# Optimization experiments

Hardware: AMD Instinct MI355X
Metric: run time of the kernel (lower is better)

Reference implementation:

```python
import jax, jax.numpy as jnp
import numpy as np

B, S, D = 1, 2048, 4096
HQ, HK, HD = 32, 8, 128


def setup_inputs() -> dict:
    key = jax.random.key(0)
    ks = jax.random.split(key, 6)
    x = jax.random.normal(ks[0], (B, S, D), jnp.float32) * 0.02
    wq = jax.random.normal(ks[1], (D, HQ * HD), jnp.float32) * 0.02
    wk = jax.random.normal(ks[2], (D, HK * HD), jnp.float32) * 0.02
    wv = jax.random.normal(ks[3], (D, HK * HD), jnp.float32) * 0.02
    wo = jax.random.normal(ks[4], (HQ * HD, D), jnp.float32) * 0.02
    # canonical RoPE frequencies: theta = 10000
    inv_freq = 1.0 / (10000.0 ** (jnp.arange(0, HD, 2, dtype=jnp.float32) / HD))  # [HD/2]
    t = jnp.arange(S, dtype=jnp.float32)
    ang = jnp.outer(t, inv_freq)  # [S, HD/2]
    return {
        "x": x,
        "freqs_cos": jnp.cos(ang),
        "freqs_sin": jnp.sin(ang),
        "wq": wq, "wk": wk, "wv": wv, "wo": wo,
    }


def _rope(t, cos, sin):
    # t: [B, S, H, HD]; pairs are consecutive elements (view_as_complex semantics)
    tr = t.reshape(*t.shape[:-1], HD // 2, 2)
    t0, t1 = tr[..., 0], tr[..., 1]
    c = cos[None, :, None, :]
    s = sin[None, :, None, :]
    o0 = t0 * c - t1 * s
    o1 = t0 * s + t1 * c
    return jnp.stack([o0, o1], axis=-1).reshape(t.shape)


def reference(x, freqs_cos, freqs_sin, wq, wk, wv, wo):
    b, s, _ = x.shape
    g = HQ // HK  # GQA group size
    xq = (x @ wq).reshape(b, s, HQ, HD)
    xk = (x @ wk).reshape(b, s, HK, HD)
    xv = (x @ wv).reshape(b, s, HK, HD)
    xq = _rope(xq, freqs_cos, freqs_sin)
    xk = _rope(xk, freqs_cos, freqs_sin)
    scale = 1.0 / jnp.sqrt(jnp.float32(HD))
    xqg = xq.reshape(b, s, HK, g, HD)
    # scores: [b, HK, g, s_q, s_k]
    scores = jnp.einsum("bqkgd,bnkd->bkgqn", xqg, xk) * scale
    causal = jnp.tril(jnp.ones((s, s), dtype=bool))
    scores = jnp.where(causal[None, None, None, :, :], scores, -jnp.inf)
    p = jax.nn.softmax(scores, axis=-1)
    out = jnp.einsum("bkgqn,bnkd->bqkgd", p, xv).reshape(b, s, HQ * HD)
    return out @ wo
```

## Files before the change

kernel.cpp:

```cpp
#include <hip/hip_runtime.h>
#include <stdint.h>

typedef __bf16 bf16_t;
typedef bf16_t bf16x8 __attribute__((ext_vector_type(8)));
typedef float f32x4 __attribute__((ext_vector_type(4)));
typedef unsigned int u32;
typedef unsigned short u16;

#define DEV_INLINE __device__ __forceinline__

#define S_LEN 2048
#define D_MODEL 4096
#define HQ 32
#define HK 8
#define HD 128
#define NQKV 6144

DEV_INLINE u16 f2bf(float x) {
  union { float f; uint32_t u; } v; v.f = x;
  uint32_t r = v.u + 0x7FFFu + ((v.u >> 16) & 1u);
  return (u16)(r >> 16);
}
DEV_INLINE float bf2f(u16 x) {
  union { uint32_t u; float f; } v; v.u = ((uint32_t)x) << 16;
  return v.f;
}
DEV_INLINE u32 pack2bf(float a, float b) {
  return (u32)f2bf(a) | ((u32)f2bf(b) << 16);
}

DEV_INLINE void async_load16(const void* g, void* l) {
  __builtin_amdgcn_global_load_lds(
      (const __attribute__((address_space(1))) u32*)g,
      (__attribute__((address_space(3))) u32*)l, 16, 0, 0);
}

DEV_INLINE f32x4 mfma16(bf16x8 a, bf16x8 b, f32x4 c) {
  return __builtin_amdgcn_mfma_f32_16x16x32_bf16(a, b, c, 0, 0, 0);
}

__global__ void cvt_f32_bf16(const float* __restrict__ in, u16* __restrict__ out, int n) {
  int i = (blockIdx.x * blockDim.x + threadIdx.x) * 4;
  if (i >= n) return;
  float4 v = *(const float4*)(in + i);
  union { u16 s[4]; uint2 u; } o;
  o.s[0] = f2bf(v.x); o.s[1] = f2bf(v.y); o.s[2] = f2bf(v.z); o.s[3] = f2bf(v.w);
  *(uint2*)(out + i) = o.u;
}

__global__ void transpose_f32_bf16(const float* __restrict__ in, u16* __restrict__ out,
                                   int R, int C) {
  __shared__ float tile[32][33];
  int tx = threadIdx.x, ty = threadIdx.y;
  int c0 = blockIdx.x * 32, r0 = blockIdx.y * 32;
#pragma unroll
  for (int i = 0; i < 4; ++i)
    tile[ty + i * 8][tx] = in[(long)(r0 + ty + i * 8) * C + c0 + tx];
  __syncthreads();
#pragma unroll
  for (int i = 0; i < 4; ++i)
    out[(long)(c0 + ty + i * 8) * R + r0 + tx] = f2bf(tile[tx][ty + i * 8]);
}

__global__ void transpose_bf16(const u16* __restrict__ in, u16* __restrict__ out,
                               int R, int C, int ld_in, int col_off) {
  __shared__ u16 tile[32][33];
  int tx = threadIdx.x, ty = threadIdx.y;
  int c0 = blockIdx.x * 32, r0 = blockIdx.y * 32;
#pragma unroll
  for (int i = 0; i < 4; ++i)
    tile[ty + i * 8][tx] = in[(long)(r0 + ty + i * 8) * ld_in + col_off + c0 + tx];
  __syncthreads();
#pragma unroll
  for (int i = 0; i < 4; ++i)
    out[(long)(c0 + ty + i * 8) * R + r0 + tx] = tile[tx][ty + i * 8];
}

__global__ void rope_bf16(const u16* __restrict__ in, const float* __restrict__ cosb,
                          const float* __restrict__ sinb, u16* __restrict__ out,
                          int H, int ld_in, int col_off, float scale) {
  int idx = blockIdx.x * blockDim.x + threadIdx.x;
  int j = idx & 63;
  int sh = idx >> 6;
  int s = sh / H, h = sh - s * H;
  const u16* ip = in + (long)s * ld_in + col_off + h * HD;
  union { u32 u; u16 s2[2]; } v; v.u = *(const u32*)(ip + 2 * j);
  float q0 = bf2f(v.s2[0]), q1 = bf2f(v.s2[1]);
  float c = cosb[s * 64 + j], sn = sinb[s * 64 + j];
  union { u16 s2[2]; u32 u; } o;
  o.s2[0] = f2bf((q0 * c - q1 * sn) * scale);
  o.s2[1] = f2bf((q0 * sn + q1 * c) * scale);
  *(u32*)(out + (long)sh * HD + 2 * j) = o.u;
}

#define BARRIER() asm volatile("s_barrier" ::: "memory")
#define WAIT_LGKM0()                                            \
  do {                                                          \
    asm volatile("s_waitcnt lgkmcnt(0)" ::: "memory");          \
    __builtin_amdgcn_sched_barrier(0);                          \
  } while (0)
#define WAIT_VM(N) asm volatile("s_waitcnt vmcnt(" #N ")" ::: "memory")

#define PHASE_A(T, DO_STAGE)                                                      \
  {                                                                               \
    const u16* Ab_ = &lds[(T) & 3][0];                                            \
    const u16* Bb_ = &lds[(T) & 3][8192];                                         \
    bf16x8 af_[MFH];                                                              \
    _Pragma("unroll")                                                             \
    for (int i = 0; i < MFH; ++i) af_[i] = rdfrag(Ab_, wr * MROWS + i * 16 + l15);\
    _Pragma("unroll")                                                             \
    for (int j = 0; j < 4; ++j) bfr[j] = rdfrag(Bb_, wc * 64 + j * 16 + l15);     \
    if (DO_STAGE) stageA((T) + 3);                                                \
    BARRIER();                                                                    \
    WAIT_LGKM0();                                                                 \
    __builtin_amdgcn_s_setprio(1);                                                \
    _Pragma("unroll")                                                             \
    for (int i = 0; i < MFH; ++i)                                                 \
      _Pragma("unroll")                                                           \
      for (int j = 0; j < 4; ++j) acc[i][j] = mfma16(af_[i], bfr[j], acc[i][j]);  \
    __builtin_amdgcn_s_setprio(0);                                                \
    BARRIER();                                                                    \
  }

#define PHASE_B(T, DO_STAGE, VMWAIT)                                              \
  {                                                                               \
    const u16* Ab_ = &lds[(T) & 3][0];                                            \
    bf16x8 af_[MFH];                                                              \
    _Pragma("unroll")                                                             \
    for (int i = 0; i < MFH; ++i)                                                 \
      af_[i] = rdfrag(Ab_, wr * MROWS + (MFH + i) * 16 + l15);                    \
    if (DO_STAGE) stageB((T) + 3);                                                \
    BARRIER();                                                                    \
    WAIT_LGKM0();                                                                 \
    __builtin_amdgcn_s_setprio(1);                                                \
    _Pragma("unroll")                                                             \
    for (int i = 0; i < MFH; ++i)                                                 \
      _Pragma("unroll")                                                           \
      for (int j = 0; j < 4; ++j)                                                 \
        acc[MFH + i][j] = mfma16(af_[i], bfr[j], acc[MFH + i][j]);                \
    __builtin_amdgcn_s_setprio(0);                                                \
    VMWAIT;                                                                       \
    BARRIER();                                                                    \
  }

template <int BN, int WM, bool BF16OUT>
__global__ __launch_bounds__(512, 2) void gemm_pipe(
    const u16* __restrict__ A, const u16* __restrict__ Bt, void* __restrict__ Cv,
    int N, int K) {
  constexpr int WN = 8 / WM;
  constexpr int MROWS = 256 / WM;
  constexpr int MF = MROWS / 16;
  constexpr int MFH = MF / 2;
  constexpr int BPT = (BN * 4) / 512;
  constexpr int LDSU = (256 + BN) * 32;

  __shared__ __attribute__((aligned(16))) u16 lds[4][LDSU];

  const int tid = threadIdx.x;
  const int lane = tid & 63;
  const int wave = tid >> 6;
  const int quad = lane >> 4, l15 = lane & 15;
  const int wr = wave / WN, wc = wave % WN;

  const int gx = gridDim.x;
  const int bid = blockIdx.y * gx + blockIdx.x;
  const int cpx = (gx * gridDim.y) >> 3;
  const int sw = (bid & 7) * cpx + (bid >> 3);
  const int bn = sw % gx, bm = sw / gx;

  const long arow = (long)bm * 256, brow = (long)bn * BN;
  const int NT = K >> 5;

  auto stageA = [&](int ts) {
    const int bs = ts & 3;
    const int k0 = ts * 32;
#pragma unroll
    for (int j = 0; j < 2; ++j) {
      int c = tid + j * 512;
      int row = c >> 2, cc = c & 3, cs = cc ^ ((row >> 1) & 3);
      async_load16(A + (arow + row) * (long)K + k0 + cs * 8,
                   (u16*)&lds[bs][0] + c * 8);
    }
  };
  auto stageB = [&](int ts) {
    const int bs = ts & 3;
    const int k0 = ts * 32;
#pragma unroll
    for (int j = 0; j < BPT; ++j) {
      int c = tid + j * 512;
      int row = c >> 2, cc = c & 3, cs = cc ^ ((row >> 1) & 3);
      async_load16(Bt + (brow + row) * (long)K + k0 + cs * 8,
                   (u16*)&lds[bs][8192] + c * 8);
    }
  };
  auto rdfrag = [&](const u16* base, int row) -> bf16x8 {
    return *(const bf16x8*)(base + row * 32 + ((quad ^ ((row >> 1) & 3)) * 8));
  };

  f32x4 acc[MF][4] = {};
  bf16x8 bfr[4];

  stageA(0); stageB(0); stageA(1); stageB(1); stageA(2); stageB(2);
  if constexpr (BN == 256) { WAIT_VM(8); } else { WAIT_VM(6); }
  BARRIER();

  int t = 0;
  for (; t < NT - 3; ++t) {
    PHASE_A(t, true);
    if constexpr (BN == 256) { PHASE_B(t, true, WAIT_VM(8)); }
    else                     { PHASE_B(t, true, WAIT_VM(6)); }
  }
  PHASE_A(t, false);
  if constexpr (BN == 256) { PHASE_B(t, false, WAIT_VM(4)); }
  else                     { PHASE_B(t, false, WAIT_VM(3)); }
  ++t;
  PHASE_A(t, false);
  PHASE_B(t, false, WAIT_VM(0));
  ++t;
  PHASE_A(t, false);
  PHASE_B(t, false, ((void)0));

#pragma unroll
  for (int i = 0; i < MF; ++i) {
    const long row = (long)bm * 256 + wr * MROWS + i * 16 + quad * 4;
#pragma unroll
    for (int j = 0; j < 4; ++j) {
      const int col = bn * BN + wc * 64 + j * 16 + l15;
      if constexpr (BF16OUT) {
        u16* C = (u16*)Cv;
#pragma unroll
        for (int r = 0; r < 4; ++r) C[(row + r) * N + col] = f2bf(acc[i][j][r]);
      } else {
        float* C = (float*)Cv;
#pragma unroll
        for (int r = 0; r < 4; ++r) C[(row + r) * N + col] = acc[i][j][r];
      }
    }
  }
}

#define NEG_INF -1e30f
__global__ __launch_bounds__(256, 2) void attn_fwd(
    const u16* __restrict__ Qb, const u16* __restrict__ Kb,
    const u16* __restrict__ Vt, u16* __restrict__ Ob) {
  __shared__ __attribute__((aligned(16))) u16 Ks[128 * 128];
  __shared__ __attribute__((aligned(16))) u16 Vs[128 * 128];
  __shared__ __attribute__((aligned(16))) u16 Pts[4][16 * 128];
  const int tid = threadIdx.x;
  const int lane = tid & 63, wave = tid >> 6;
  const int quad = lane >> 4, l15 = lane & 15;
  const int u = 15 - blockIdx.x;
  const int h = blockIdx.y, hk = h >> 2;
  const int swz = 2 * (l15 & 7);

  bf16x8 qf[2][4];
#pragma unroll
  for (int n = 0; n < 2; ++n) {
    const u16* qrow = Qb + (long)(u * 128 + wave * 32 + n * 16 + l15) * (HQ * HD)
                      + h * HD + quad * 8;
#pragma unroll
    for (int ks = 0; ks < 4; ++ks) qf[n][ks] = *(const bf16x8*)(qrow + ks * 32);
  }

  float m_run[2] = {NEG_INF, NEG_INF}, l_run[2] = {0.f, 0.f};
  f32x4 oacc[8][2] = {};

  for (int j = 0; j <= u; ++j) {
#pragma unroll
    for (int it = 0; it < 8; ++it) {
      int c = tid + it * 256;
      int row = c >> 4, cc = c & 15, csrc = cc ^ (row & 15);
      async_load16(Kb + (long)(j * 128 + row) * (HK * HD) + hk * HD + csrc * 8,
                   (u16*)Ks + c * 8);
      async_load16(Vt + (long)(hk * HD + row) * S_LEN + j * 128 + csrc * 8,
                   (u16*)Vs + c * 8);
    }
    __syncthreads();

    f32x4 sc[8][2] = {};
#pragma unroll
    for (int ks = 0; ks < 4; ++ks)
#pragma unroll
      for (int tj = 0; tj < 8; ++tj) {
        int row = tj * 16 + l15;
        bf16x8 kf = *(const bf16x8*)(Ks + row * 128 + (((ks * 4 + quad) ^ (row & 15)) * 8));
        sc[tj][0] = mfma16(kf, qf[0][ks], sc[tj][0]);
        sc[tj][1] = mfma16(kf, qf[1][ks], sc[tj][1]);
      }

    const bool diag = (j == u);
#pragma unroll
    for (int n = 0; n < 2; ++n) {
      int qloc = wave * 32 + n * 16 + l15;
      if (diag) {
#pragma unroll
        for (int tj = 0; tj < 8; ++tj)
#pragma unroll
          for (int r = 0; r < 4; ++r)
            if (tj * 16 + quad * 4 + r > qloc) sc[tj][n][r] = NEG_INF;
      }
      float m = NEG_INF;
#pragma unroll
      for (int tj = 0; tj < 8; ++tj)
#pragma unroll
        for (int r = 0; r < 4; ++r) m = fmaxf(m, sc[tj][n][r]);
      m = fmaxf(m, __shfl_xor(m, 16));
      m = fmaxf(m, __shfl_xor(m, 32));
      float mnew = fmaxf(m_run[n], m);
      float alpha = __expf(m_run[n] - mnew);
      m_run[n] = mnew;
      float rs = 0.f;
#pragma unroll
      for (int tj = 0; tj < 8; ++tj)
#pragma unroll
        for (int r = 0; r < 4; ++r) {
          float p = __expf(sc[tj][n][r] - mnew);
          sc[tj][n][r] = p;
          rs += p;
        }
      rs += __shfl_xor(rs, 16);
      rs += __shfl_xor(rs, 32);
      l_run[n] = l_run[n] * alpha + rs;
#pragma unroll
      for (int tj = 0; tj < 8; ++tj) oacc[tj][n] *= alpha;
    }

    u16* pw = &Pts[wave][0];
    bf16x8 pf0[4], pf1[4];
#pragma unroll
    for (int tj = 0; tj < 8; ++tj) {
      union { u32 w[2]; uint2 u2; } pk;
      pk.w[0] = pack2bf(sc[tj][0][0], sc[tj][0][1]);
      pk.w[1] = pack2bf(sc[tj][0][2], sc[tj][0][3]);
      *(uint2*)(pw + l15 * 128 + (((tj * 4 + quad) ^ swz) * 4)) = pk.u2;
    }
    __asm__ volatile("s_waitcnt lgkmcnt(0)" ::: "memory");
#pragma unroll
    for (int ks = 0; ks < 4; ++ks)
      pf0[ks] = *(const bf16x8*)(pw + l15 * 128 + (((ks * 8 + quad * 2) ^ swz) * 4));
    __asm__ volatile("s_waitcnt lgkmcnt(0)" ::: "memory");
#pragma unroll
    for (int tj = 0; tj < 8; ++tj) {
      union { u32 w[2]; uint2 u2; } pk;
      pk.w[0] = pack2bf(sc[tj][1][0], sc[tj][1][1]);
      pk.w[1] = pack2bf(sc[tj][1][2], sc[tj][1][3]);
      *(uint2*)(pw + l15 * 128 + (((tj * 4 + quad) ^ swz) * 4)) = pk.u2;
    }
    __asm__ volatile("s_waitcnt lgkmcnt(0)" ::: "memory");
#pragma unroll
    for (int ks = 0; ks < 4; ++ks)
      pf1[ks] = *(const bf16x8*)(pw + l15 * 128 + (((ks * 8 + quad * 2) ^ swz) * 4));

#pragma unroll
    for (int ks = 0; ks < 4; ++ks)
#pragma unroll
      for (int tj = 0; tj < 8; ++tj) {
        int row = tj * 16 + l15;
        bf16x8 vf = *(const bf16x8*)(Vs + row * 128 + (((ks * 4 + quad) ^ (row & 15)) * 8));
        oacc[tj][0] = mfma16(vf, pf0[ks], oacc[tj][0]);
        oacc[tj][1] = mfma16(vf, pf1[ks], oacc[tj][1]);
      }
    __syncthreads();
  }

#pragma unroll
  for (int n = 0; n < 2; ++n) {
    float inv_l = 1.0f / l_run[n];
    long grow = u * 128 + wave * 32 + n * 16 + l15;
#pragma unroll
    for (int tj = 0; tj < 8; ++tj) {
      int gcol = h * HD + tj * 16 + quad * 4;
      union { u32 w[2]; uint2 u2; } pk;
      pk.w[0] = pack2bf(oacc[tj][n][0] * inv_l, oacc[tj][n][1] * inv_l);
      pk.w[1] = pack2bf(oacc[tj][n][2] * inv_l, oacc[tj][n][3] * inv_l);
      *(uint2*)(Ob + grow * (HQ * HD) + gcol) = pk.u2;
    }
  }
}

#define MB (1024L * 1024L)

extern "C" void kernel_launch(void* const* d_in, const int* in_sizes, int n_in,
                              void* d_out, int out_size, void* d_ws, size_t ws_size,
                              hipStream_t stream) {
  const float* x    = (const float*)d_in[0];
  const float* fcos = (const float*)d_in[1];
  const float* fsin = (const float*)d_in[2];
  const float* wq   = (const float*)d_in[3];
  const float* wk   = (const float*)d_in[4];
  const float* wv   = (const float*)d_in[5];
  const float* wo   = (const float*)d_in[6];
  float* out = (float*)d_out;

  char* ws = (char*)d_ws;
  u16* wt    = (u16*)(ws + 0 * MB);
  u16* xb    = (u16*)(ws + 48 * MB);
  u16* QKVb  = (u16*)(ws + 64 * MB);
  u16* Qb    = (u16*)(ws + 88 * MB);
  u16* Kb    = (u16*)(ws + 104 * MB);
  u16* Vt    = (u16*)(ws + 108 * MB);
  u16* attnb = (u16*)(ws + 112 * MB);

  const int M = S_LEN, D = D_MODEL;

  cvt_f32_bf16<<<(M * D) / 1024, 256, 0, stream>>>(x, xb, M * D);

  transpose_f32_bf16<<<dim3(D / 32, D / 32), dim3(32, 8), 0, stream>>>(wq, wt, D, HQ * HD);
  transpose_f32_bf16<<<dim3((HK * HD) / 32, D / 32), dim3(32, 8), 0, stream>>>(
      wk, wt + (long)(HQ * HD) * D, D, HK * HD);
  transpose_f32_bf16<<<dim3((HK * HD) / 32, D / 32), dim3(32, 8), 0, stream>>>(
      wv, wt + (long)(HQ * HD + HK * HD) * D, D, HK * HD);

  gemm_pipe<256, 2, true><<<dim3(NQKV / 256, M / 256), 512, 0, stream>>>(
      xb, wt, QKVb, NQKV, D);

  rope_bf16<<<(M * HQ * 64) / 256, 256, 0, stream>>>(
      QKVb, fcos, fsin, Qb, HQ, NQKV, 0, 0.08838834764831845f);
  rope_bf16<<<(M * HK * 64) / 256, 256, 0, stream>>>(
      QKVb, fcos, fsin, Kb, HK, NQKV, HQ * HD, 1.0f);
  transpose_bf16<<<dim3((HK * HD) / 32, M / 32), dim3(32, 8), 0, stream>>>(
      QKVb, Vt, M, HK * HD, NQKV, HQ * HD + HK * HD);

  attn_fwd<<<dim3(16, HQ), 256, 0, stream>>>(Qb, Kb, Vt, attnb);

  transpose_f32_bf16<<<dim3(D / 32, D / 32), dim3(32, 8), 0, stream>>>(wo, wt, HQ * HD, D);
  gemm_pipe<128, 4, false><<<dim3(D / 128, M / 256), 512, 0, stream>>>(
      attnb, wt, out, D, HQ * HD);
}
```

Baseline: 541.7 us.

## Double-buffer 64-wide KV tiles, skip masked waves, lazy rescale, balance block order

Shrinks the attention KV tile from 128 to 64 keys and double-buffers K and V in shared memory, so the async load of the next tile overlaps compute on the current one. Waves whose query rows lie entirely before the current key tile skip its work. The online softmax rescales only when the max grows by more than a threshold (lazy rescaling), and MFMA sections are wrapped in s_setprio. Block indices are remapped so heads interleave and causal row-blocks pair long with short. This adds a loop iteration per 64 keys, more barriers, and relies on exp(8) headroom for accuracy.

```diff
diff --git a/kernel.cpp b/kernel.cpp
--- a/kernel.cpp
+++ b/kernel.cpp
@@ -243,15 +243,19 @@
 __global__ __launch_bounds__(256, 2) void attn_fwd(
     const u16* __restrict__ Qb, const u16* __restrict__ Kb,
     const u16* __restrict__ Vt, u16* __restrict__ Ob) {
-  __shared__ __attribute__((aligned(16))) u16 Ks[128 * 128];
-  __shared__ __attribute__((aligned(16))) u16 Vs[128 * 128];
-  __shared__ __attribute__((aligned(16))) u16 Pts[4][16 * 128];
+  __shared__ __attribute__((aligned(16))) u16 Ks[2][64 * 128];
+  __shared__ __attribute__((aligned(16))) u16 Vs[2][128 * 64];
+  __shared__ __attribute__((aligned(16))) u16 Pts[4][16 * 64];
   const int tid = threadIdx.x;
   const int lane = tid & 63, wave = tid >> 6;
   const int quad = lane >> 4, l15 = lane & 15;
-  const int u = 15 - blockIdx.x;
-  const int h = blockIdx.y, hk = h >> 2;
+  const int lin = blockIdx.y * gridDim.x + blockIdx.x;
+  const int h = lin & 31;
+  const int pp = (lin >> 5) & 7;
+  const int u = (lin >> 8) ? 15 - pp : pp;
+  const int hk = h >> 2;
   const int swz = 2 * (l15 & 7);
+  const int nt = 2 * (u + 1);
 
   bf16x8 qf[2][4];
 #pragma unroll
@@ -262,104 +266,130 @@
     for (int ks = 0; ks < 4; ++ks) qf[n][ks] = *(const bf16x8*)(qrow + ks * 32);
   }
 
+  auto stage = [&](int t) {
+    const int b = t & 1;
+#pragma unroll
+    for (int it = 0; it < 4; ++it) {
+      int c = tid + it * 256;
+      int row = c >> 4, cc = c & 15, cs = cc ^ (row & 15);
+      async_load16(Kb + (long)(t * 64 + row) * (HK * HD) + hk * HD + cs * 8,
+                   (u16*)&Ks[b][0] + c * 8);
+    }
+#pragma unroll
+    for (int it = 0; it < 4; ++it) {
+      int c = tid + it * 256;
+      int row = c >> 3, cc = c & 7, cs = cc ^ (row & 7);
+      async_load16(Vt + (long)(hk * HD + row) * S_LEN + t * 64 + cs * 8,
+                   (u16*)&Vs[b][0] + c * 8);
+    }
+  };
+
   float m_run[2] = {NEG_INF, NEG_INF}, l_run[2] = {0.f, 0.f};
   f32x4 oacc[8][2] = {};
 
-  for (int j = 0; j <= u; ++j) {
-#pragma unroll
-    for (int it = 0; it < 8; ++it) {
-      int c = tid + it * 256;
-      int row = c >> 4, cc = c & 15, csrc = cc ^ (row & 15);
-      async_load16(Kb + (long)(j * 128 + row) * (HK * HD) + hk * HD + csrc * 8,
-                   (u16*)Ks + c * 8);
-      async_load16(Vt + (long)(hk * HD + row) * S_LEN + j * 128 + csrc * 8,
-                   (u16*)Vs + c * 8);
-    }
-    __syncthreads();
-
-    f32x4 sc[8][2] = {};
-#pragma unroll
-    for (int ks = 0; ks < 4; ++ks)
-#pragma unroll
-      for (int tj = 0; tj < 8; ++tj) {
-        int row = tj * 16 + l15;
-        bf16x8 kf = *(const bf16x8*)(Ks + row * 128 + (((ks * 4 + quad) ^ (row & 15)) * 8));
-        sc[tj][0] = mfma16(kf, qf[0][ks], sc[tj][0]);
-        sc[tj][1] = mfma16(kf, qf[1][ks], sc[tj][1]);
+  stage(0);
+  __syncthreads();
+
+  for (int t = 0; t < nt; ++t) {
+    const int cur = t & 1;
+    if (t + 1 < nt) stage(t + 1);
+
+    if (t * 64 <= u * 128 + wave * 32 + 31) {
+      f32x4 sc[4][2] = {};
+      __builtin_amdgcn_s_setprio(1);
+#pragma unroll
+      for (int ks = 0; ks < 4; ++ks)
+#pragma unroll
+        for (int tj = 0; tj < 4; ++tj) {
+          int row = tj * 16 + l15;
+          bf16x8 kf = *(const bf16x8*)(&Ks[cur][0] + row * 128
+                                       + (((ks * 4 + quad) ^ (row & 15)) * 8));
+          sc[tj][0] = mfma16(kf, qf[0][ks], sc[tj][0]);
+          sc[tj][1] = mfma16(kf, qf[1][ks], sc[tj][1]);
+        }
+      __builtin_amdgcn_s_setprio(0);
+
+      const bool diag = (t >= 2 * u);
+      const int kbase = t * 64 - u * 128;
+#pragma unroll
+      for (int n = 0; n < 2; ++n) {
+        int qloc = wave * 32 + n * 16 + l15;
+        if (diag) {
+#pragma unroll
+          for (int tj = 0; tj < 4; ++tj)
+#pragma unroll
+            for (int r = 0; r < 4; ++r)
+              if (kbase + tj * 16 + quad * 4 + r > qloc) sc[tj][n][r] = NEG_INF;
+        }
+        float m = NEG_INF;
+#pragma unroll
+        for (int tj = 0; tj < 4; ++tj)
+#pragma unroll
+          for (int r = 0; r < 4; ++r) m = fmaxf(m, sc[tj][n][r]);
+        m = fmaxf(m, __shfl_xor(m, 16));
+        m = fmaxf(m, __shfl_xor(m, 32));
+        if (!__all(m - m_run[n] <= 8.0f)) {
+          float mnew = fmaxf(m_run[n], m);
+          float alpha = __expf(m_run[n] - mnew);
+          m_run[n] = mnew;
+          l_run[n] *= alpha;
+#pragma unroll
+          for (int tj = 0; tj < 8; ++tj) oacc[tj][n] *= alpha;
+        }
+        float rs = 0.f;
+#pragma unroll
+        for (int tj = 0; tj < 4; ++tj)
+#pragma unroll
+          for (int r = 0; r < 4; ++r) {
+            float p = __expf(sc[tj][n][r] - m_run[n]);
+            sc[tj][n][r] = p;
+            rs += p;
+          }
+        rs += __shfl_xor(rs, 16);
+        rs += __shfl_xor(rs, 32);
+        l_run[n] += rs;
       }
 
-    const bool diag = (j == u);
-#pragma unroll
-    for (int n = 0; n < 2; ++n) {
-      int qloc = wave * 32 + n * 16 + l15;
-      if (diag) {
-#pragma unroll
-        for (int tj = 0; tj < 8; ++tj)
-#pragma unroll
-          for (int r = 0; r < 4; ++r)
-            if (tj * 16 + quad * 4 + r > qloc) sc[tj][n][r] = NEG_INF;
+      u16* pw = &Pts[wave][0];
+      bf16x8 pf0[2], pf1[2];
+#pragma unroll
+      for (int tj = 0; tj < 4; ++tj) {
+        union { u32 w[2]; uint2 u2; } pk;
+        pk.w[0] = pack2bf(sc[tj][0][0], sc[tj][0][1]);
+        pk.w[1] = pack2bf(sc[tj][0][2], sc[tj][0][3]);
+        *(uint2*)(pw + l15 * 64 + (((tj * 4 + quad) ^ swz) * 4)) = pk.u2;
       }
-      float m = NEG_INF;
-#pragma unroll
-      for (int tj = 0; tj < 8; ++tj)
-#pragma unroll
-        for (int r = 0; r < 4; ++r) m = fmaxf(m, sc[tj][n][r]);
-      m = fmaxf(m, __shfl_xor(m, 16));
-      m = fmaxf(m, __shfl_xor(m, 32));
-      float mnew = fmaxf(m_run[n], m);
-      float alpha = __expf(m_run[n] - mnew);
-      m_run[n] = mnew;
-      float rs = 0.f;
-#pragma unroll
-      for (int tj = 0; tj < 8; ++tj)
-#pragma unroll
-        for (int r = 0; r < 4; ++r) {
-          float p = __expf(sc[tj][n][r] - mnew);
-          sc[tj][n][r] = p;
-          rs += p;
+      __asm__ volatile("s_waitcnt lgkmcnt(0)" ::: "memory");
+#pragma unroll
+      for (int ks = 0; ks < 2; ++ks)
+        pf0[ks] = *(const bf16x8*)(pw + l15 * 64 + (((ks * 8 + quad * 2) ^ swz) * 4));
+      __asm__ volatile("s_waitcnt lgkmcnt(0)" ::: "memory");
+#pragma unroll
+      for (int tj = 0; tj < 4; ++tj) {
+        union { u32 w[2]; uint2 u2; } pk;
+        pk.w[0] = pack2bf(sc[tj][1][0], sc[tj][1][1]);
+        pk.w[1] = pack2bf(sc[tj][1][2], sc[tj][1][3]);
+        *(uint2*)(pw + l15 * 64 + (((tj * 4 + quad) ^ swz) * 4)) = pk.u2;
+      }
+      __asm__ volatile("s_waitcnt lgkmcnt(0)" ::: "memory");
+#pragma unroll
+      for (int ks = 0; ks < 2; ++ks)
+        pf1[ks] = *(const bf16x8*)(pw + l15 * 64 + (((ks * 8 + quad * 2) ^ swz) * 4));
+
+      __builtin_amdgcn_s_setprio(1);
+#pragma unroll
+      for (int ks = 0; ks < 2; ++ks)
+#pragma unroll
+        for (int tj = 0; tj < 8; ++tj) {
+          int row = tj * 16 + l15;
+          bf16x8 vf = *(const bf16x8*)(&Vs[cur][0] + row * 64
+                                       + (((ks * 4 + quad) ^ (row & 7)) * 8));
+          oacc[tj][0] = mfma16(vf, pf0[ks], oacc[tj][0]);
+          oacc[tj][1] = mfma16(vf, pf1[ks], oacc[tj][1]);
         }
-      rs += __shfl_xor(rs, 16);
-      rs += __shfl_xor(rs, 32);
-      l_run[n] = l_run[n] * alpha + rs;
-#pragma unroll
-      for (int tj = 0; tj < 8; ++tj) oacc[tj][n] *= alpha;
-    }
-
-    u16* pw = &Pts[wave][0];
-    bf16x8 pf0[4], pf1[4];
-#pragma unroll
-    for (int tj = 0; tj < 8; ++tj) {
-      union { u32 w[2]; uint2 u2; } pk;
-      pk.w[0] = pack2bf(sc[tj][0][0], sc[tj][0][1]);
-      pk.w[1] = pack2bf(sc[tj][0][2], sc[tj][0][3]);
-      *(uint2*)(pw + l15 * 128 + (((tj * 4 + quad) ^ swz) * 4)) = pk.u2;
-    }
-    __asm__ volatile("s_waitcnt lgkmcnt(0)" ::: "memory");
-#pragma unroll
-    for (int ks = 0; ks < 4; ++ks)
-      pf0[ks] = *(const bf16x8*)(pw + l15 * 128 + (((ks * 8 + quad * 2) ^ swz) * 4));
-    __asm__ volatile("s_waitcnt lgkmcnt(0)" ::: "memory");
-#pragma unroll
-    for (int tj = 0; tj < 8; ++tj) {
-      union { u32 w[2]; uint2 u2; } pk;
-      pk.w[0] = pack2bf(sc[tj][1][0], sc[tj][1][1]);
-      pk.w[1] = pack2bf(sc[tj][1][2], sc[tj][1][3]);
-      *(uint2*)(pw + l15 * 128 + (((tj * 4 + quad) ^ swz) * 4)) = pk.u2;
-    }
-    __asm__ volatile("s_waitcnt lgkmcnt(0)" ::: "memory");
-#pragma unroll
-    for (int ks = 0; ks < 4; ++ks)
-      pf1[ks] = *(const bf16x8*)(pw + l15 * 128 + (((ks * 8 + quad * 2) ^ swz) * 4));
-
-#pragma unroll
-    for (int ks = 0; ks < 4; ++ks)
-#pragma unroll
-      for (int tj = 0; tj < 8; ++tj) {
-        int row = tj * 16 + l15;
-        bf16x8 vf = *(const bf16x8*)(Vs + row * 128 + (((ks * 4 + quad) ^ (row & 15)) * 8));
-        oacc[tj][0] = mfma16(vf, pf0[ks], oacc[tj][0]);
-        oacc[tj][1] = mfma16(vf, pf1[ks], oacc[tj][1]);
-      }
+      __builtin_amdgcn_s_setprio(0);
+    }
+
     __syncthreads();
   }
 
```

After: 493.5 us. -8.9%, faster.
